# Kernel tuning notes

Measured on AMD Instinct MI355X. Metric: run time of the kernel, lower is better.

Reference implementation:

```python
import jax, jax.numpy as jnp
import numpy as np

K = 3          # kernel size
PAD = 1        # (K-1)//2, stride=1, dilation=1


def _modulated_deform_conv(depth, offset, mask, w, b):
    """torchvision deform_conv2d with in_ch=out_ch=1, stride=1, pad=1, dil=1.
    depth:  [B,1,H,W]
    offset: [B,2*K*K,H,W]  interleaved (dy, dx) per kernel tap
    mask:   [B,K*K,H,W]    modulation scalars
    w:      [1,1,K,K]      conv weights (ones buffer)
    b:      [1]            bias (zeros buffer)
    """
    B, _, H, W = depth.shape
    kk = K * K
    img = depth[:, 0]                                    # [B,H,W]

    off = offset.reshape(B, kk, 2, H, W)
    dy, dx = off[:, :, 0], off[:, :, 1]                  # [B,kk,H,W]

    # integer tap offsets of the 3x3 kernel
    ky, kx = jnp.meshgrid(jnp.arange(K), jnp.arange(K), indexing='ij')
    ky = ky.reshape(kk).astype(depth.dtype)
    kx = kx.reshape(kk).astype(depth.dtype)

    iy = jnp.arange(H, dtype=depth.dtype)
    ix = jnp.arange(W, dtype=depth.dtype)
    # sampling coords per output pixel per tap: [B,kk,H,W]
    y = iy[None, None, :, None] - PAD + ky[None, :, None, None] + dy
    x = ix[None, None, None, :] - PAD + kx[None, :, None, None] + dx

    y0f = jnp.floor(y); x0f = jnp.floor(x)
    wy = y - y0f; wx = x - x0f                           # frac parts
    y0 = y0f.astype(jnp.int32); x0 = x0f.astype(jnp.int32)
    y1 = y0 + 1;  x1 = x0 + 1

    bidx = jnp.arange(B)[:, None, None, None]

    def corner(yc, xc):
        inb = (yc >= 0) & (yc < H) & (xc >= 0) & (xc < W)
        v = img[bidx, jnp.clip(yc, 0, H - 1), jnp.clip(xc, 0, W - 1)]
        return jnp.where(inb, v, jnp.zeros((), depth.dtype))

    sampled = (corner(y0, x0) * (1 - wy) * (1 - wx)
             + corner(y0, x1) * (1 - wy) * wx
             + corner(y1, x0) * wy * (1 - wx)
             + corner(y1, x1) * wy * wx)                 # [B,kk,H,W]

    wk = w.reshape(1, kk, 1, 1)
    out = jnp.sum(sampled * mask * wk, axis=1) + b[0]    # [B,H,W]
    return out[:, None]                                  # [B,1,H,W]


def setup_inputs() -> dict:
    key = jax.random.key(0)
    k1, k2, k3 = jax.random.split(key, 3)
    B, H, W = 8, 512, 512
    depth  = jax.random.normal(k1, (B, 1, H, W), dtype=jnp.float32)
    weight = jax.random.uniform(k2, (B, K * K, H, W), dtype=jnp.float32)
    offset = jax.random.normal(k3, (B, 2 * K * K, H, W), dtype=jnp.float32)
    w = jnp.ones((1, 1, K, K), dtype=jnp.float32)   # buffer 'w'
    b = jnp.zeros((1,), dtype=jnp.float32)          # buffer 'b'
    return {"depth": depth, "weight": weight, "offset": offset, "w": w, "b": b}


def reference(depth, weight, offset, w, b):
    return _modulated_deform_conv(depth, offset, weight, w, b)
```

## Files before the change

kernel.cpp:

```cpp
#include <hip/hip_runtime.h>


#define KK 9
#define PAD 1
#define H 512
#define W 512
#define HW (H * W)

#define TX 64
#define TY 8
#define HALO 8
#define LWL (TX + 2 * HALO)
#define LH  (TY + 2 * HALO)
#define LWS (LWL + 1)
#define SAFE ((LH - 2) * LWS + (LWL - 2))

typedef float f2 __attribute__((ext_vector_type(2)));

__device__ __forceinline__ float bilin_global(const float* __restrict__ img,
                                              float y, float x) {
    float y0f = floorf(y);
    float x0f = floorf(x);
    int y0 = (int)y0f;
    int x0 = (int)x0f;
    float wy = y - y0f;
    float wx = x - x0f;
    int y1 = y0 + 1;
    int x1 = x0 + 1;

    bool y0i = (y0 >= 0) & (y0 < H);
    bool y1i = (y1 >= 0) & (y1 < H);
    bool x0i = (x0 >= 0) & (x0 < W);
    bool x1i = (x1 >= 0) & (x1 < W);

    int y0c = min(max(y0, 0), H - 1);
    int y1c = min(max(y1, 0), H - 1);
    int x0c = min(max(x0, 0), W - 1);
    int x1c = min(max(x1, 0), W - 1);

    float v00 = (y0i & x0i) ? img[y0c * W + x0c] : 0.0f;
    float v01 = (y0i & x1i) ? img[y0c * W + x1c] : 0.0f;
    float v10 = (y1i & x0i) ? img[y1c * W + x0c] : 0.0f;
    float v11 = (y1i & x1i) ? img[y1c * W + x1c] : 0.0f;

    float omwy = 1.0f - wy;
    float omwx = 1.0f - wx;
    return fmaf(v00 * omwy, omwx,
           fmaf(v01 * omwy, wx,
           fmaf(v10 * wy,   omwx, v11 * wy * wx)));
}

__device__ __forceinline__ float sample_nb(const float* S, float syr, float sxr,
                                           int& oob) {
    const float y0f = floorf(syr);
    const float x0f = floorf(sxr);
    const float wy = syr - y0f;
    const float wx = sxr - x0f;
    const int ly = (int)y0f;
    const int lx = (int)x0f;
    oob |= (int)(((unsigned)ly >= (unsigned)(LH - 1)) |
                 ((unsigned)lx >= (unsigned)(LWL - 1)));
    unsigned su = (unsigned)(ly * LWS + lx);
    su = su < (unsigned)SAFE ? su : (unsigned)SAFE;
    const float v00 = S[su];
    const float v01 = S[su + 1];
    const float v10 = S[su + LWS];
    const float v11 = S[su + LWS + 1];
    const float omwy = 1.0f - wy;
    const float omwx = 1.0f - wx;
    return fmaf(v00 * omwy, omwx,
           fmaf(v01 * omwy, wx,
           fmaf(v10 * wy,   omwx, v11 * wy * wx)));
}

__global__ __launch_bounds__(256, 5) void dcn_kernel(
    const float* __restrict__ depth,
    const float* __restrict__ mask,
    const float* __restrict__ offset,
    const float* __restrict__ w9,
    const float* __restrict__ bias,
    float* __restrict__ out) {
    __shared__ float S[LH * LWS];

    const int b  = blockIdx.z;
    const int bx = blockIdx.x;
    const int by = blockIdx.y;
    const int tX0 = bx * TX - HALO;
    const int tY0 = by * TY - HALO;

    const float* __restrict__ img = depth + (long)b * HW;

    const int xp = threadIdx.x & 31;
    const int yr = threadIdx.x >> 5;
    const int tx = bx * TX + 2 * xp;
    const int ty = by * TY + yr;
    const int pix = ty * W + tx;

    const float* __restrict__ msk = mask   + ((long)b * KK)     * HW + pix;
    const float* __restrict__ off = offset + ((long)b * 2 * KK) * HW + pix;

    f2 dy0, dy1, dy2, dy3, dy4, dy5, dy6, dy7, dy8;
    f2 dx0, dx1, dx2, dx3, dx4, dx5, dx6, dx7, dx8;
    f2 m0, m1, m2, m3, m4, m5, m6, m7, m8;
#define LDT(k)                                              \
    dy##k = *(const f2*)(off + (2 * k) * HW);               \
    dx##k = *(const f2*)(off + (2 * k + 1) * HW);           \
    m##k  = *(const f2*)(msk + k * HW);
    LDT(0) LDT(1) LDT(2) LDT(3) LDT(4) LDT(5) LDT(6) LDT(7) LDT(8)
#undef LDT
    __builtin_amdgcn_sched_barrier(0);

    for (int i = threadIdx.x; i < LH * LWL; i += 256) {
        const int ly = i / LWL;
        const int lx = i - ly * LWL;
        const int gy = tY0 + ly;
        const int gx = tX0 + lx;
        float v = 0.0f;
        if (((unsigned)gy < (unsigned)H) & ((unsigned)gx < (unsigned)W))
            v = img[gy * W + gx];
        S[ly * LWS + lx] = v;
    }
    __syncthreads();

    const float bs = bias[0];
    float a0 = bs, a1 = bs;
    int oob = 0;
    const float sybr = (float)(yr + HALO - PAD);
    const float sxbr = (float)(2 * xp + HALO - PAD);

#define CTAP(k, KYC, KXC)                                                     \
    {                                                                         \
        const float wk = w9[k];                                               \
        const float syA = sybr + (float)(KYC) + dy##k.x;                      \
        const float sxA = sxbr + (float)(KXC) + dx##k.x;                      \
        a0 = fmaf(sample_nb(S, syA, sxA, oob), m##k.x * wk, a0);              \
        const float syB = sybr + (float)(KYC) + dy##k.y;                      \
        const float sxB = sxbr + (float)(KXC) + 1.0f + dx##k.y;               \
        a1 = fmaf(sample_nb(S, syB, sxB, oob), m##k.y * wk, a1);              \
    }
    CTAP(0, 0, 0) CTAP(1, 0, 1) CTAP(2, 0, 2)
    CTAP(3, 1, 0) CTAP(4, 1, 1) CTAP(5, 1, 2)
    CTAP(6, 2, 0) CTAP(7, 2, 1) CTAP(8, 2, 2)
#undef CTAP

    if (__builtin_expect(__any(oob), 0)) {
        if (oob) {
            a0 = bs;
            a1 = bs;
#pragma unroll 1
            for (int k = 0; k < KK; ++k) {
                const int ky = k / 3;
                const int kx = k - 3 * ky;
                const float wk = w9[k];
                const float fdy0 = off[(2 * k) * HW];
                const float fdy1 = off[(2 * k) * HW + 1];
                const float fdx0 = off[(2 * k + 1) * HW];
                const float fdx1 = off[(2 * k + 1) * HW + 1];
                const float fm0 = msk[k * HW];
                const float fm1 = msk[k * HW + 1];
                const float syA = (float)(ty - PAD + ky) + fdy0;
                const float sxA = (float)(tx - PAD + kx) + fdx0;
                a0 = fmaf(bilin_global(img, syA, sxA), fm0 * wk, a0);
                const float syB = (float)(ty - PAD + ky) + fdy1;
                const float sxB = (float)(tx - PAD + kx + 1) + fdx1;
                a1 = fmaf(bilin_global(img, syB, sxB), fm1 * wk, a1);
            }
        }
    }

    f2 r;
    r.x = a0;
    r.y = a1;
    *(f2*)(out + (long)b * HW + pix) = r;
}

extern "C" void kernel_launch(void* const* d_in, const int* in_sizes, int n_in,
                              void* d_out, int out_size, void* d_ws, size_t ws_size,
                              hipStream_t stream) {
    const float* depth  = (const float*)d_in[0];
    const float* mask   = (const float*)d_in[1];
    const float* offset = (const float*)d_in[2];
    const float* w9     = (const float*)d_in[3];
    const float* bias   = (const float*)d_in[4];
    float* out = (float*)d_out;

    const int B = in_sizes[0] / HW;

    dim3 block(256);
    dim3 grid(W / TX, H / TY, B);
    dcn_kernel<<<grid, block, 0, stream>>>(depth, mask, offset, w9, bias, out);
}
```

Before: 274.5 us.

## Process four pixels per thread with taller tiles and vectorized halo loads

Each thread now computes four adjacent output pixels instead of two, using float4 loads for offsets, masks and the output, and the tile height doubles to 16 rows. The shared-memory halo fill switches to float4 global loads with a padded row stride of 84, and surplus chunks go to a trash slot. This cuts the halo overhead per output and the number of memory instructions, at the cost of more registers (launch bounds drop to 4 blocks per CU) and possible LDS bank conflicts from the new stride.

```diff
diff --git a/kernel.cpp b/kernel.cpp
--- a/kernel.cpp
+++ b/kernel.cpp
@@ -8,14 +8,17 @@
 #define HW (H * W)
 
 #define TX 64
-#define TY 8
+#define TY 16
 #define HALO 8
 #define LWL (TX + 2 * HALO)
 #define LH  (TY + 2 * HALO)
-#define LWS (LWL + 1)
+#define LWS 84
+#define NCHUNK (LH * LWL / 4)
 #define SAFE ((LH - 2) * LWS + (LWL - 2))
+#define TRASH (LH * LWS)
 
 typedef float f2 __attribute__((ext_vector_type(2)));
+typedef float f4 __attribute__((ext_vector_type(4)));
 
 __device__ __forceinline__ float bilin_global(const float* __restrict__ img,
                                               float y, float x) {
@@ -73,14 +76,14 @@
            fmaf(v10 * wy,   omwx, v11 * wy * wx)));
 }
 
-__global__ __launch_bounds__(256, 5) void dcn_kernel(
+__global__ __launch_bounds__(256, 4) void dcn_kernel(
     const float* __restrict__ depth,
     const float* __restrict__ mask,
     const float* __restrict__ offset,
     const float* __restrict__ w9,
     const float* __restrict__ bias,
     float* __restrict__ out) {
-    __shared__ float S[LH * LWS];
+    __shared__ float S[LH * LWS + 4];
 
     const int b  = blockIdx.z;
     const int bx = blockIdx.x;
@@ -90,88 +93,103 @@
 
     const float* __restrict__ img = depth + (long)b * HW;
 
-    const int xp = threadIdx.x & 31;
-    const int yr = threadIdx.x >> 5;
-    const int tx = bx * TX + 2 * xp;
+    const int xq = threadIdx.x & 15;
+    const int yr = threadIdx.x >> 4;
+    const int tx = bx * TX + 4 * xq;
     const int ty = by * TY + yr;
     const int pix = ty * W + tx;
 
     const float* __restrict__ msk = mask   + ((long)b * KK)     * HW + pix;
     const float* __restrict__ off = offset + ((long)b * 2 * KK) * HW + pix;
 
-    f2 dy0, dy1, dy2, dy3, dy4, dy5, dy6, dy7, dy8;
-    f2 dx0, dx1, dx2, dx3, dx4, dx5, dx6, dx7, dx8;
-    f2 m0, m1, m2, m3, m4, m5, m6, m7, m8;
+    const float wk0 = w9[0], wk1 = w9[1], wk2 = w9[2];
+    const float wk3 = w9[3], wk4 = w9[4], wk5 = w9[5];
+    const float wk6 = w9[6], wk7 = w9[7], wk8 = w9[8];
+    const float bs = bias[0];
+
+    f4 dy0, dy1, dy2, dy3, dy4, dy5, dy6, dy7, dy8;
+    f4 dx0, dx1, dx2, dx3, dx4, dx5, dx6, dx7, dx8;
+    f4 m0, m1, m2, m3, m4, m5, m6, m7, m8;
 #define LDT(k)                                              \
-    dy##k = *(const f2*)(off + (2 * k) * HW);               \
-    dx##k = *(const f2*)(off + (2 * k + 1) * HW);           \
-    m##k  = *(const f2*)(msk + k * HW);
+    dy##k = *(const f4*)(off + (2 * k) * HW);               \
+    dx##k = *(const f4*)(off + (2 * k + 1) * HW);           \
+    m##k  = *(const f4*)(msk + k * HW);
     LDT(0) LDT(1) LDT(2) LDT(3) LDT(4) LDT(5) LDT(6) LDT(7) LDT(8)
 #undef LDT
-    __builtin_amdgcn_sched_barrier(0);
-
-    for (int i = threadIdx.x; i < LH * LWL; i += 256) {
-        const int ly = i / LWL;
-        const int lx = i - ly * LWL;
-        const int gy = tY0 + ly;
-        const int gx = tX0 + lx;
-        float v = 0.0f;
-        if (((unsigned)gy < (unsigned)H) & ((unsigned)gx < (unsigned)W))
-            v = img[gy * W + gx];
-        S[ly * LWS + lx] = v;
+
+    #pragma unroll
+    for (int j = 0; j < 3; ++j) {
+        const int c   = (int)threadIdx.x + j * 256;
+        const int ly  = c / 20;
+        const int lx4 = (c - ly * 20) * 4;
+        const int gy  = tY0 + ly;
+        const int gx  = tX0 + lx4;
+        const int ok  = (int)(((unsigned)gy < (unsigned)H) &
+                              ((unsigned)gx < (unsigned)W));
+        const f4 v = *(const f4*)(img + (ok ? (gy * W + gx) : 0));
+        f4 z;
+        z.x = ok ? v.x : 0.0f;
+        z.y = ok ? v.y : 0.0f;
+        z.z = ok ? v.z : 0.0f;
+        z.w = ok ? v.w : 0.0f;
+        const int si = (c < NCHUNK) ? (ly * LWS + lx4) : TRASH;
+        *(f4*)(S + si) = z;
     }
     __syncthreads();
 
-    const float bs = bias[0];
-    float a0 = bs, a1 = bs;
+    float a0 = bs, a1 = bs, a2 = bs, a3 = bs;
     int oob = 0;
     const float sybr = (float)(yr + HALO - PAD);
-    const float sxbr = (float)(2 * xp + HALO - PAD);
-
-#define CTAP(k, KYC, KXC)                                                     \
-    {                                                                         \
-        const float wk = w9[k];                                               \
-        const float syA = sybr + (float)(KYC) + dy##k.x;                      \
-        const float sxA = sxbr + (float)(KXC) + dx##k.x;                      \
-        a0 = fmaf(sample_nb(S, syA, sxA, oob), m##k.x * wk, a0);              \
-        const float syB = sybr + (float)(KYC) + dy##k.y;                      \
-        const float sxB = sxbr + (float)(KXC) + 1.0f + dx##k.y;               \
-        a1 = fmaf(sample_nb(S, syB, sxB, oob), m##k.y * wk, a1);              \
+    const float sxbr = (float)(4 * xq + HALO - PAD);
+
+#define CTAP(k, KYC, KXC, WK)                                                  \
+    {                                                                          \
+        const float syk = sybr + (float)(KYC);                                 \
+        const float sxk = sxbr + (float)(KXC);                                 \
+        a0 = fmaf(sample_nb(S, syk + dy##k.x, sxk + 0.0f + dx##k.x, oob),      \
+                  m##k.x * (WK), a0);                                          \
+        a1 = fmaf(sample_nb(S, syk + dy##k.y, sxk + 1.0f + dx##k.y, oob),      \
+                  m##k.y * (WK), a1);                                          \
+        a2 = fmaf(sample_nb(S, syk + dy##k.z, sxk + 2.0f + dx##k.z, oob),      \
+                  m##k.z * (WK), a2);                                          \
+        a3 = fmaf(sample_nb(S, syk + dy##k.w, sxk + 3.0f + dx##k.w, oob),      \
+                  m##k.w * (WK), a3);                                          \
     }
-    CTAP(0, 0, 0) CTAP(1, 0, 1) CTAP(2, 0, 2)
-    CTAP(3, 1, 0) CTAP(4, 1, 1) CTAP(5, 1, 2)
-    CTAP(6, 2, 0) CTAP(7, 2, 1) CTAP(8, 2, 2)
+    CTAP(0, 0, 0, wk0) CTAP(1, 0, 1, wk1) CTAP(2, 0, 2, wk2)
+    CTAP(3, 1, 0, wk3) CTAP(4, 1, 1, wk4) CTAP(5, 1, 2, wk5)
+    CTAP(6, 2, 0, wk6) CTAP(7, 2, 1, wk7) CTAP(8, 2, 2, wk8)
 #undef CTAP
 
     if (__builtin_expect(__any(oob), 0)) {
         if (oob) {
-            a0 = bs;
-            a1 = bs;
+            a0 = bs; a1 = bs; a2 = bs; a3 = bs;
 #pragma unroll 1
             for (int k = 0; k < KK; ++k) {
                 const int ky = k / 3;
                 const int kx = k - 3 * ky;
                 const float wk = w9[k];
-                const float fdy0 = off[(2 * k) * HW];
-                const float fdy1 = off[(2 * k) * HW + 1];
-                const float fdx0 = off[(2 * k + 1) * HW];
-                const float fdx1 = off[(2 * k + 1) * HW + 1];
-                const float fm0 = msk[k * HW];
-                const float fm1 = msk[k * HW + 1];
-                const float syA = (float)(ty - PAD + ky) + fdy0;
-                const float sxA = (float)(tx - PAD + kx) + fdx0;
-                a0 = fmaf(bilin_global(img, syA, sxA), fm0 * wk, a0);
-                const float syB = (float)(ty - PAD + ky) + fdy1;
-                const float sxB = (float)(tx - PAD + kx + 1) + fdx1;
-                a1 = fmaf(bilin_global(img, syB, sxB), fm1 * wk, a1);
+                const float syb = (float)(ty - PAD + ky);
+                const float sxb = (float)(tx - PAD + kx);
+#pragma unroll 1
+                for (int p = 0; p < 4; ++p) {
+                    const float fdy = off[(2 * k) * HW + p];
+                    const float fdx = off[(2 * k + 1) * HW + p];
+                    const float fm  = msk[k * HW + p];
+                    const float sv  = bilin_global(img, syb + fdy,
+                                                   sxb + (float)p + fdx);
+                    const float add = sv * fm * wk;
+                    a0 += (p == 0) ? add : 0.0f;
+                    a1 += (p == 1) ? add : 0.0f;
+                    a2 += (p == 2) ? add : 0.0f;
+                    a3 += (p == 3) ? add : 0.0f;
+                }
             }
         }
     }
 
-    f2 r;
-    r.x = a0;
-    r.y = a1;
-    *(f2*)(out + (long)b * HW + pix) = r;
+    f4 r;
+    r.x = a0; r.y = a1; r.z = a2; r.w = a3;
+    *(f4*)(out + (long)b * HW + pix) = r;
 }
 
 extern "C" void kernel_launch(void* const* d_in, const int* in_sizes, int n_in,
```

After: 280.6 us. 1.02x slower.

## Use full-width row tiles with vectorized LDS staging and zero-padded columns

Applied to the files above, without the earlier changes.

Each block now covers a full 512-wide strip of two output rows with 512 threads. It stages 18 image rows into LDS using float4 loads, with padded zero columns so horizontal bounds checks become one range test. This removes horizontal halo redundancy and scalar staging loads. The cost is a much larger vertical halo ratio (18 rows loaded for 2 output rows), a bigger LDS footprint that may limit occupancy, and the removal of the sched_barrier that overlapped offset loads with staging.

```diff
diff --git a/kernel.cpp b/kernel.cpp
--- a/kernel.cpp
+++ b/kernel.cpp
@@ -7,15 +7,12 @@
 #define W 512
 #define HW (H * W)
 
-#define TX 64
-#define TY 8
-#define HALO 8
-#define LWL (TX + 2 * HALO)
-#define LH  (TY + 2 * HALO)
-#define LWS (LWL + 1)
-#define SAFE ((LH - 2) * LWS + (LWL - 2))
+#define STRIDE 520
+#define LROWS 18
+#define SAFE 8835u
 
 typedef float f2 __attribute__((ext_vector_type(2)));
+typedef float f4 __attribute__((ext_vector_type(4)));
 
 __device__ __forceinline__ float bilin_global(const float* __restrict__ img,
                                               float y, float x) {
@@ -50,22 +47,22 @@
            fmaf(v10 * wy,   omwx, v11 * wy * wx)));
 }
 
-__device__ __forceinline__ float sample_nb(const float* S, float syr, float sxr,
+__device__ __forceinline__ float sample_fw(const float* S, float syr, float sxa,
                                            int& oob) {
     const float y0f = floorf(syr);
-    const float x0f = floorf(sxr);
+    const float x0f = floorf(sxa);
     const float wy = syr - y0f;
-    const float wx = sxr - x0f;
+    const float wx = sxa - x0f;
     const int ly = (int)y0f;
-    const int lx = (int)x0f;
-    oob |= (int)(((unsigned)ly >= (unsigned)(LH - 1)) |
-                 ((unsigned)lx >= (unsigned)(LWL - 1)));
-    unsigned su = (unsigned)(ly * LWS + lx);
-    su = su < (unsigned)SAFE ? su : (unsigned)SAFE;
+    const int x0 = (int)x0f;
+    oob |= (int)(((unsigned)ly >= (unsigned)(LROWS - 1)) |
+                 ((unsigned)(x0 + 1) >= 513u));
+    unsigned su = (unsigned)(ly * STRIDE + 4 + x0);
+    su = su < SAFE ? su : SAFE;
     const float v00 = S[su];
     const float v01 = S[su + 1];
-    const float v10 = S[su + LWS];
-    const float v11 = S[su + LWS + 1];
+    const float v10 = S[su + STRIDE];
+    const float v11 = S[su + STRIDE + 1];
     const float omwy = 1.0f - wy;
     const float omwx = 1.0f - wx;
     return fmaf(v00 * omwy, omwx,
@@ -73,74 +70,87 @@
            fmaf(v10 * wy,   omwx, v11 * wy * wx)));
 }
 
-__global__ __launch_bounds__(256, 5) void dcn_kernel(
+__global__ __launch_bounds__(512, 8) void dcn_kernel(
     const float* __restrict__ depth,
     const float* __restrict__ mask,
     const float* __restrict__ offset,
     const float* __restrict__ w9,
     const float* __restrict__ bias,
     float* __restrict__ out) {
-    __shared__ float S[LH * LWS];
+    __shared__ float S[LROWS * STRIDE];
 
     const int b  = blockIdx.z;
-    const int bx = blockIdx.x;
     const int by = blockIdx.y;
-    const int tX0 = bx * TX - HALO;
-    const int tY0 = by * TY - HALO;
+    const int tY0 = 2 * by - 8;
 
     const float* __restrict__ img = depth + (long)b * HW;
-
-    const int xp = threadIdx.x & 31;
-    const int yr = threadIdx.x >> 5;
-    const int tx = bx * TX + 2 * xp;
-    const int ty = by * TY + yr;
+    const int tid = (int)threadIdx.x;
+
+    #pragma unroll
+    for (int j = 0; j < 5; ++j) {
+        const int c = tid + j * 512;
+        if (c < LROWS * 128) {
+            const int ly = c >> 7;
+            const int cx = (c & 127) << 2;
+            const int gy = tY0 + ly;
+            const int ok = (int)((unsigned)gy < (unsigned)H);
+            const f4 v = *(const f4*)(img + (ok ? (gy * W + cx) : 0));
+            f4 z;
+            z.x = ok ? v.x : 0.0f;
+            z.y = ok ? v.y : 0.0f;
+            z.z = ok ? v.z : 0.0f;
+            z.w = ok ? v.w : 0.0f;
+            *(f4*)(S + ly * STRIDE + 4 + cx) = z;
+        }
+    }
+    if (tid < 2 * LROWS) {
+        const int r = tid >> 1;
+        S[r * STRIDE + ((tid & 1) ? 516 : 3)] = 0.0f;
+    }
+
+    const int xp = tid & 255;
+    const int yr = tid >> 8;
+    const int tx = 2 * xp;
+    const int ty = 2 * by + yr;
     const int pix = ty * W + tx;
 
-    const float* __restrict__ msk = mask   + ((long)b * KK)     * HW + pix;
-    const float* __restrict__ off = offset + ((long)b * 2 * KK) * HW + pix;
+    const float* __restrict__ mskp = mask   + ((long)b * KK)     * HW + pix;
+    const float* __restrict__ offp = offset + ((long)b * 2 * KK) * HW + pix;
 
     f2 dy0, dy1, dy2, dy3, dy4, dy5, dy6, dy7, dy8;
     f2 dx0, dx1, dx2, dx3, dx4, dx5, dx6, dx7, dx8;
     f2 m0, m1, m2, m3, m4, m5, m6, m7, m8;
-#define LDT(k)                                              \
-    dy##k = *(const f2*)(off + (2 * k) * HW);               \
-    dx##k = *(const f2*)(off + (2 * k + 1) * HW);           \
-    m##k  = *(const f2*)(msk + k * HW);
+#define LDT(k)                                               \
+    dy##k = *(const f2*)(offp + (2 * k) * HW);               \
+    dx##k = *(const f2*)(offp + (2 * k + 1) * HW);           \
+    m##k  = *(const f2*)(mskp + k * HW);
     LDT(0) LDT(1) LDT(2) LDT(3) LDT(4) LDT(5) LDT(6) LDT(7) LDT(8)
 #undef LDT
-    __builtin_amdgcn_sched_barrier(0);
-
-    for (int i = threadIdx.x; i < LH * LWL; i += 256) {
-        const int ly = i / LWL;
-        const int lx = i - ly * LWL;
-        const int gy = tY0 + ly;
-        const int gx = tX0 + lx;
-        float v = 0.0f;
-        if (((unsigned)gy < (unsigned)H) & ((unsigned)gx < (unsigned)W))
-            v = img[gy * W + gx];
-        S[ly * LWS + lx] = v;
-    }
+
+    const float wk0 = w9[0], wk1 = w9[1], wk2 = w9[2];
+    const float wk3 = w9[3], wk4 = w9[4], wk5 = w9[5];
+    const float wk6 = w9[6], wk7 = w9[7], wk8 = w9[8];
+    const float bs = bias[0];
+
     __syncthreads();
 
-    const float bs = bias[0];
     float a0 = bs, a1 = bs;
     int oob = 0;
-    const float sybr = (float)(yr + HALO - PAD);
-    const float sxbr = (float)(2 * xp + HALO - PAD);
-
-#define CTAP(k, KYC, KXC)                                                     \
+    const float sybr = (float)(yr + 7);
+    const float sxbr = (float)(tx - 1);
+
+#define CTAP(k, KYC, KXC, WK)                                                 \
     {                                                                         \
-        const float wk = w9[k];                                               \
-        const float syA = sybr + (float)(KYC) + dy##k.x;                      \
-        const float sxA = sxbr + (float)(KXC) + dx##k.x;                      \
-        a0 = fmaf(sample_nb(S, syA, sxA, oob), m##k.x * wk, a0);              \
-        const float syB = sybr + (float)(KYC) + dy##k.y;                      \
-        const float sxB = sxbr + (float)(KXC) + 1.0f + dx##k.y;               \
-        a1 = fmaf(sample_nb(S, syB, sxB, oob), m##k.y * wk, a1);              \
-    }
-    CTAP(0, 0, 0) CTAP(1, 0, 1) CTAP(2, 0, 2)
-    CTAP(3, 1, 0) CTAP(4, 1, 1) CTAP(5, 1, 2)
-    CTAP(6, 2, 0) CTAP(7, 2, 1) CTAP(8, 2, 2)
+        const float syk = sybr + (float)(KYC);                                \
+        const float sxk = sxbr + (float)(KXC);                                \
+        a0 = fmaf(sample_fw(S, syk + dy##k.x, sxk + 0.0f + dx##k.x, oob),     \
+                  m##k.x * (WK), a0);                                         \
+        a1 = fmaf(sample_fw(S, syk + dy##k.y, sxk + 1.0f + dx##k.y, oob),     \
+                  m##k.y * (WK), a1);                                         \
+    }
+    CTAP(0, 0, 0, wk0) CTAP(1, 0, 1, wk1) CTAP(2, 0, 2, wk2)
+    CTAP(3, 1, 0, wk3) CTAP(4, 1, 1, wk4) CTAP(5, 1, 2, wk5)
+    CTAP(6, 2, 0, wk6) CTAP(7, 2, 1, wk7) CTAP(8, 2, 2, wk8)
 #undef CTAP
 
     if (__builtin_expect(__any(oob), 0)) {
@@ -152,12 +162,12 @@
                 const int ky = k / 3;
                 const int kx = k - 3 * ky;
                 const float wk = w9[k];
-                const float fdy0 = off[(2 * k) * HW];
-                const float fdy1 = off[(2 * k) * HW + 1];
-                const float fdx0 = off[(2 * k + 1) * HW];
-                const float fdx1 = off[(2 * k + 1) * HW + 1];
-                const float fm0 = msk[k * HW];
-                const float fm1 = msk[k * HW + 1];
+                const float fdy0 = offp[(2 * k) * HW];
+                const float fdy1 = offp[(2 * k) * HW + 1];
+                const float fdx0 = offp[(2 * k + 1) * HW];
+                const float fdx1 = offp[(2 * k + 1) * HW + 1];
+                const float fm0 = mskp[k * HW];
+                const float fm1 = mskp[k * HW + 1];
                 const float syA = (float)(ty - PAD + ky) + fdy0;
                 const float sxA = (float)(tx - PAD + kx) + fdx0;
                 a0 = fmaf(bilin_global(img, syA, sxA), fm0 * wk, a0);
@@ -186,7 +196,7 @@
 
     const int B = in_sizes[0] / HW;
 
-    dim3 block(256);
-    dim3 grid(W / TX, H / TY, B);
+    dim3 block(512);
+    dim3 grid(1, H / 2, B);
     dcn_kernel<<<grid, block, 0, stream>>>(depth, mask, offset, w9, bias, out);
 }
```

Result: slower. 307.8 us (+12.1%).
